# Performance work log

Measured on AMD Instinct MI355X. Metric: run time of the kernel, lower is better.

Reference implementation:

```python
import jax, jax.numpy as jnp
import numpy as np
from jax import lax

SEQ_LEN = 5000
C_IN = 12
KERNEL_LEN = 9
NUM_KERNELS = 10000
BATCH = 16


def _get_dilations(seq_len, kernel_length):
    max_d = (seq_len - 1) // (kernel_length - 1)
    d, out = 1, []
    while d <= max_d:
        out.append(d)
        d *= 2
    return out if out else [1]

DILATIONS = _get_dilations(SEQ_LEN, KERNEL_LEN)  # [1,2,...,512], 10 dilations
KPD = NUM_KERNELS // len(DILATIONS)              # 1000 kernels per dilation


def setup_inputs() -> dict:
    key = jax.random.key(0)
    kx, kw, kb = jax.random.split(key, 3)
    x = jax.random.normal(kx, (BATCH, C_IN, SEQ_LEN), dtype=jnp.float32)
    # ternary {-1,0,1} MiniRocket weights, one [KPD, C_IN, 9] bank per dilation
    weights = jax.random.randint(kw, (len(DILATIONS), KPD, C_IN, KERNEL_LEN), -1, 2).astype(jnp.float32)
    biases = jax.random.normal(kb, (len(DILATIONS), KPD), dtype=jnp.float32) * 0.1
    return {"x": x, "weights": weights, "biases": biases}


def reference(x, weights, biases):
    # x: [B, C_in, L]; weights: [D, KPD, C_in, 9]; biases: [D, KPD]
    feats = []
    for i, d in enumerate(DILATIONS):
        # 'same' padding: total pad = d*(9-1) = 8d (even), split 4d/4d -> SAME
        out = lax.conv_general_dilated(
            x, weights[i],
            window_strides=(1,), padding='SAME', rhs_dilation=(d,),
            dimension_numbers=('NCH', 'OIH', 'NCH'))  # [B, KPD, L]
        maxv = out.max(axis=-1)                                        # [B, KPD]
        ppv = (out > biases[i][None, :, None]).astype(x.dtype).mean(axis=-1)  # [B, KPD]
        feats.append(maxv)
        feats.append(ppv)
    return jnp.concatenate(feats, axis=1)  # [B, 2*NUM_KERNELS]
```

## Files before the change

### kernel.cpp

```cpp
#include <hip/hip_runtime.h>
#include <cstdint>
#include <cstddef>

#define SEQ 5000
#define CIN 12
#define KL 9
#define ND 10
#define KPD 1000
#define NB 16
#define KPAD 128
#define NKP 1024
#define BM 64
#define SPB 79
#define STRIP_US (BM * KPAD)
#define QS 20

typedef __attribute__((ext_vector_type(4))) float f32x4;
typedef __attribute__((ext_vector_type(8))) __bf16 bf16x8;
typedef __attribute__((ext_vector_type(8))) unsigned short u16x8;

__device__ __forceinline__ unsigned fkey(float f) {
    unsigned u = __float_as_uint(f);
    return (u & 0x80000000u) ? ~u : (u | 0x80000000u);
}
__device__ __forceinline__ float unfkey(unsigned k) {
    unsigned u = (k & 0x80000000u) ? (k ^ 0x80000000u) : ~k;
    return __uint_as_float(u);
}
__device__ __forceinline__ unsigned short f2bf(float f) {
    unsigned u = __float_as_uint(f);
    u += 0x7fffu + ((u >> 16) & 1u);
    return (unsigned short)(u >> 16);
}

__global__ __launch_bounds__(256) void wprep(const float* __restrict__ w,
                                             unsigned short* __restrict__ wbf) {
    const int i = blockIdx.x * 256 + threadIdx.x;
    if (i >= ND * NKP * KPAD) return;
    const int kk   = i & (KPAD - 1);
    const int krow = (i >> 7) & (NKP - 1);
    const int di   = i >> 17;
    float v = 0.f;
    if (krow < KPD && kk < CIN * KL)
        v = w[((size_t)di * KPD + krow) * (CIN * KL) + kk];
    wbf[i] = f2bf(v);
}

__global__ __launch_bounds__(256) void im2col(const float* __restrict__ x,
                                              unsigned short* __restrict__ Aim,
                                              int g0) {
    const int s  = blockIdx.x;
    const int b  = blockIdx.y;
    const int dl = blockIdx.z;
    const int d  = 1 << (g0 + dl);
    const int tid  = threadIdx.x;
    const int lane = tid & 63;
    const int wv   = tid >> 6;

    __shared__ __align__(16) unsigned short sb[STRIP_US];

    const float* xb = x + (size_t)b * CIN * SEQ;
    const int t0 = s * BM;
    const int t  = t0 + lane;
    const int base = t - 4 * d;
    const bool rowvalid = (t < SEQ);

#pragma unroll
    for (int cwi = 0; cwi < 4; ++cwi) {
        const int cw = wv * 4 + cwi;
        u16x8 pk;
        int cc = cw * 8;
        int c = cc / 9, j = cc - c * 9;
#pragma unroll
        for (int e = 0; e < 8; ++e) {
            const int idx = base + j * d;
            float v = 0.f;
            if (rowvalid && cc < CIN * KL && idx >= 0 && idx < SEQ)
                v = xb[c * SEQ + idx];
            pk[e] = f2bf(v);
            ++cc; if (++j == KL) { j = 0; ++c; }
        }
        *(u16x8*)(sb + lane * KPAD + ((cw * 8) ^ ((lane & 7) << 3))) = pk;
    }
    __syncthreads();

    unsigned short* outp = Aim + ((size_t)(dl * NB + b) * SPB + s) * STRIP_US;
#pragma unroll
    for (int i = 0; i < 4; ++i) {
        const int u = (i * 256 + tid) * 8;
        *(u16x8*)(outp + u) = *(const u16x8*)(sb + u);
    }
}

__global__ __launch_bounds__(256, 4) void mr_gemm(
    const unsigned short* __restrict__ Aim,
    const unsigned short* __restrict__ wbf,
    const float* __restrict__ bias,
    unsigned* __restrict__ gkey, unsigned* __restrict__ gcnt, int g0)
{
    __shared__ __align__(16) unsigned short lA[2][STRIP_US];

    const int phys = blockIdx.x;
    const int gg   = ((phys >> 6) << 3) | (phys & 7);
    const int ksub = (phys >> 3) & 7;
    const int q  = gg & 3;
    const int b  = (gg >> 2) & 15;
    const int dl = gg >> 6;
    const int di = g0 + dl;

    const int tid  = threadIdx.x;
    const int lane = tid & 63;
    const int wv   = tid >> 6;
    const int wm   = wv >> 1;
    const int wn   = wv & 1;
    const int fr   = lane & 15;
    const int ks   = lane >> 4;

    const int sBeg = q * QS;
    const int sEnd = (q == 3) ? SPB : (sBeg + QS);

    const unsigned short* Ab = Aim + (size_t)(dl * NB + b) * SPB * STRIP_US;
    const unsigned short* wd = wbf + (size_t)di * NKP * KPAD;
    const int kcb = ksub * 128 + wn * 64 + fr;
    const unsigned short* wp = wd + (size_t)kcb * KPAD + ks * 8;
    const float* bb = bias + (size_t)di * KPD;

    float bv[4];
#pragma unroll
    for (int n = 0; n < 4; ++n) {
        const int kc = kcb + n * 16;
        bv[n] = (kc < KPD) ? bb[kc] : 3.0e38f;
    }

    bf16x8 bfr[4][4];
#pragma unroll
    for (int n = 0; n < 4; ++n)
#pragma unroll
        for (int kk = 0; kk < 4; ++kk)
            bfr[n][kk] = *(const bf16x8*)(wp + (size_t)(n * 16) * KPAD + kk * 32);

    float rmax[4];
    unsigned rcnt[4];
#pragma unroll
    for (int n = 0; n < 4; ++n) { rmax[n] = -3.0e38f; rcnt[n] = 0; }

    int abase[2];
#pragma unroll
    for (int m2 = 0; m2 < 2; ++m2) {
        const int row = wm * 32 + m2 * 16 + fr;
        abase[m2] = row * 256 + ((ks * 16) ^ ((row & 7) << 4));
    }

    {
        const char* src = (const char*)(Ab + (size_t)sBeg * STRIP_US) + wv * 4096 + lane * 16;
        char* dst = (char*)&lA[0][0] + wv * 4096;
#pragma unroll
        for (int i = 0; i < 4; ++i)
            __builtin_amdgcn_global_load_lds(
                (const __attribute__((address_space(1))) unsigned int*)(src + i * 1024),
                (__attribute__((address_space(3))) unsigned int*)(dst + i * 1024),
                16, 0, 0);
    }
    __syncthreads();

    for (int s = sBeg; s < sEnd; ++s) {
        const int cur = (s - sBeg) & 1;
        if (s + 1 < sEnd) {
            const char* src = (const char*)(Ab + (size_t)(s + 1) * STRIP_US) + wv * 4096 + lane * 16;
            char* dst = (char*)&lA[cur ^ 1][0] + wv * 4096;
#pragma unroll
            for (int i = 0; i < 4; ++i)
                __builtin_amdgcn_global_load_lds(
                    (const __attribute__((address_space(1))) unsigned int*)(src + i * 1024),
                    (__attribute__((address_space(3))) unsigned int*)(dst + i * 1024),
                    16, 0, 0);
        }

        const char* bufc = (const char*)&lA[cur][0];
        f32x4 acc[2][4];
#pragma unroll
        for (int m2 = 0; m2 < 2; ++m2)
#pragma unroll
            for (int n = 0; n < 4; ++n)
                acc[m2][n] = (f32x4){0.f, 0.f, 0.f, 0.f};

#pragma unroll
        for (int m2 = 0; m2 < 2; ++m2) {
            const char* pa0 = bufc + abase[m2];
            const char* pa1 = bufc + (abase[m2] ^ 64);
#pragma unroll
            for (int kk = 0; kk < 4; ++kk) {
                const char* p = (kk & 1) ? pa1 : pa0;
                const bf16x8 a = *(const bf16x8*)(p + (kk >> 1) * 128);
#pragma unroll
                for (int n = 0; n < 4; ++n)
                    acc[m2][n] = __builtin_amdgcn_mfma_f32_16x16x32_bf16(
                        a, bfr[n][kk], acc[m2][n], 0, 0, 0);
            }
        }

        if (s != SPB - 1) {
#pragma unroll
            for (int n = 0; n < 4; ++n) {
                float m0 = -3.0e38f;
                unsigned c0 = 0;
#pragma unroll
                for (int m2 = 0; m2 < 2; ++m2) {
#pragma unroll
                    for (int r = 0; r < 4; ++r) {
                        const float x0 = acc[m2][n][r];
                        m0 = fmaxf(m0, x0);
                        c0 += (x0 > bv[n]) ? 1u : 0u;
                    }
                }
                rmax[n] = fmaxf(rmax[n], m0);
                rcnt[n] += c0;
            }
        } else {
            if (wm == 0 && ks < 2) {
#pragma unroll
                for (int n = 0; n < 4; ++n) {
#pragma unroll
                    for (int r = 0; r < 4; ++r) {
                        const float x0 = acc[0][n][r];
                        rmax[n] = fmaxf(rmax[n], x0);
                        rcnt[n] += (x0 > bv[n]) ? 1u : 0u;
                    }
                }
            }
        }
        __syncthreads();
    }

#pragma unroll
    for (int n = 0; n < 4; ++n) {
        rmax[n] = fmaxf(rmax[n], __shfl_xor(rmax[n], 16, 64));
        rcnt[n] += (unsigned)__shfl_xor((int)rcnt[n], 16, 64);
        rmax[n] = fmaxf(rmax[n], __shfl_xor(rmax[n], 32, 64));
        rcnt[n] += (unsigned)__shfl_xor((int)rcnt[n], 32, 64);
    }

    if (lane < 16) {
        const size_t slotbase = ((size_t)b * ND + di) * KPD;
#pragma unroll
        for (int n = 0; n < 4; ++n) {
            const int kc = kcb + n * 16;
            if (kc < KPD) {
                atomicMax(&gkey[slotbase + kc], fkey(rmax[n]));
                atomicAdd(&gcnt[slotbase + kc], rcnt[n]);
            }
        }
    }
}

__global__ __launch_bounds__(256) void mr_fin(
    const unsigned* __restrict__ gkey, const unsigned* __restrict__ gcnt,
    float* __restrict__ out)
{
    const int i = blockIdx.x * 256 + threadIdx.x;
    if (i >= NB * ND * KPD) return;
    const int k  = i % KPD;
    const int di = (i / KPD) % ND;
    const int b  = i / (KPD * ND);
    const float maxv = unfkey(gkey[i]);
    const float ppv  = (float)gcnt[i] * (1.0f / (float)SEQ);
    float* ob = out + (size_t)b * (2 * ND * KPD);
    ob[di * 2 * KPD + k]       = maxv;
    ob[di * 2 * KPD + KPD + k] = ppv;
}

extern "C" void kernel_launch(void* const* d_in, const int* in_sizes, int n_in,
                              void* d_out, int out_size, void* d_ws, size_t ws_size,
                              hipStream_t stream) {
    const float* x    = (const float*)d_in[0];
    const float* w    = (const float*)d_in[1];
    const float* bias = (const float*)d_in[2];
    float* out = (float*)d_out;

    const size_t statsB = (size_t)NB * ND * KPD * 4;
    const size_t wbfB   = (size_t)ND * NKP * KPAD * 2;
    unsigned* gkey = (unsigned*)d_ws;
    unsigned* gcnt = (unsigned*)((char*)d_ws + statsB);
    unsigned short* wbf = (unsigned short*)((char*)d_ws + 2 * statsB);
    unsigned short* Aim = (unsigned short*)((char*)d_ws + 2 * statsB + wbfB);

    const size_t perDil = (size_t)NB * SPB * STRIP_US * 2;
    const size_t head = 2 * statsB + wbfB;
    size_t avail = (ws_size > head) ? (ws_size - head) : 0;
    int NG = (int)(avail / perDil);
    if (NG > ND) NG = ND;
    if (NG < 1) NG = 1;

    hipMemsetAsync(d_ws, 0, 2 * statsB, stream);

    const int wtot = ND * NKP * KPAD;
    wprep<<<(wtot + 255) / 256, 256, 0, stream>>>(w, wbf);

    for (int g0 = 0; g0 < ND; g0 += NG) {
        const int ng = (ND - g0 < NG) ? (ND - g0) : NG;
        im2col<<<dim3(SPB, NB, ng), 256, 0, stream>>>(x, Aim, g0);
        mr_gemm<<<ng * 512, 256, 0, stream>>>(Aim, wbf, bias, gkey, gcnt, g0);
    }

    const int tot = NB * ND * KPD;
    mr_fin<<<(tot + 255) / 256, 256, 0, stream>>>(gkey, gcnt, out);
}
```

Measured before the change: 276.5 us.

## Process two A strips per iteration with larger per-wave tiles, reload weights per step

The GEMM loop now stages 128-row superstrips of 32 KB instead of 64-row strips. Each wave computes 64 rows by 64 kernels using 4x4 MFMA accumulators, which raises A-fragment reuse and halves the number of loop iterations and barriers. To save registers, the bf16 weight fragments are no longer kept in registers for the whole kernel and are reloaded from global memory at every k-step. Occupancy hints drop from 4 to 2 blocks per CU. The final superstrip reads past the last real strip, so the workspace head is padded; the exchange is extra weight-load traffic and lower occupancy for better MFMA density.

Result: slower. 323.0 us (+16.8%).

```diff
diff --git a/kernel.cpp b/kernel.cpp
--- a/kernel.cpp
+++ b/kernel.cpp
@@ -13,7 +13,9 @@
 #define BM 64
 #define SPB 79
 #define STRIP_US (BM * KPAD)
-#define QS 20
+#define SS_BYTES 32768
+#define NSS 40
+#define QSS 10
 
 typedef __attribute__((ext_vector_type(4))) float f32x4;
 typedef __attribute__((ext_vector_type(8))) __bf16 bf16x8;
@@ -92,13 +94,13 @@
     }
 }
 
-__global__ __launch_bounds__(256, 4) void mr_gemm(
+__global__ __launch_bounds__(256, 2) void mr_gemm(
     const unsigned short* __restrict__ Aim,
     const unsigned short* __restrict__ wbf,
     const float* __restrict__ bias,
     unsigned* __restrict__ gkey, unsigned* __restrict__ gcnt, int g0)
 {
-    __shared__ __align__(16) unsigned short lA[2][STRIP_US];
+    __shared__ __align__(16) unsigned short lA[2][SS_BYTES / 2];
 
     const int phys = blockIdx.x;
     const int gg   = ((phys >> 6) << 3) | (phys & 7);
@@ -116,10 +118,10 @@
     const int fr   = lane & 15;
     const int ks   = lane >> 4;
 
-    const int sBeg = q * QS;
-    const int sEnd = (q == 3) ? SPB : (sBeg + QS);
-
-    const unsigned short* Ab = Aim + (size_t)(dl * NB + b) * SPB * STRIP_US;
+    const int sBeg = q * QSS;
+    const int sEnd = sBeg + QSS;
+
+    const char* Ab = (const char*)(Aim + (size_t)(dl * NB + b) * SPB * STRIP_US);
     const unsigned short* wd = wbf + (size_t)di * NKP * KPAD;
     const int kcb = ksub * 128 + wn * 64 + fr;
     const unsigned short* wp = wd + (size_t)kcb * KPAD + ks * 8;
@@ -132,80 +134,78 @@
         bv[n] = (kc < KPD) ? bb[kc] : 3.0e38f;
     }
 
-    bf16x8 bfr[4][4];
-#pragma unroll
-    for (int n = 0; n < 4; ++n)
-#pragma unroll
-        for (int kk = 0; kk < 4; ++kk)
-            bfr[n][kk] = *(const bf16x8*)(wp + (size_t)(n * 16) * KPAD + kk * 32);
-
     float rmax[4];
     unsigned rcnt[4];
 #pragma unroll
     for (int n = 0; n < 4; ++n) { rmax[n] = -3.0e38f; rcnt[n] = 0; }
 
-    int abase[2];
-#pragma unroll
-    for (int m2 = 0; m2 < 2; ++m2) {
-        const int row = wm * 32 + m2 * 16 + fr;
+    int abase[4];
+#pragma unroll
+    for (int m2 = 0; m2 < 4; ++m2) {
+        const int row = wm * 64 + m2 * 16 + fr;
         abase[m2] = row * 256 + ((ks * 16) ^ ((row & 7) << 4));
     }
 
     {
-        const char* src = (const char*)(Ab + (size_t)sBeg * STRIP_US) + wv * 4096 + lane * 16;
-        char* dst = (char*)&lA[0][0] + wv * 4096;
-#pragma unroll
-        for (int i = 0; i < 4; ++i)
+        const char* src = Ab + (size_t)sBeg * SS_BYTES + wv * 1024 + lane * 16;
+        char* dst = (char*)&lA[0][0] + wv * 1024;
+#pragma unroll
+        for (int i = 0; i < 8; ++i)
             __builtin_amdgcn_global_load_lds(
-                (const __attribute__((address_space(1))) unsigned int*)(src + i * 1024),
-                (__attribute__((address_space(3))) unsigned int*)(dst + i * 1024),
+                (const __attribute__((address_space(1))) unsigned int*)(src + i * 4096),
+                (__attribute__((address_space(3))) unsigned int*)(dst + i * 4096),
                 16, 0, 0);
     }
     __syncthreads();
 
-    for (int s = sBeg; s < sEnd; ++s) {
-        const int cur = (s - sBeg) & 1;
-        if (s + 1 < sEnd) {
-            const char* src = (const char*)(Ab + (size_t)(s + 1) * STRIP_US) + wv * 4096 + lane * 16;
-            char* dst = (char*)&lA[cur ^ 1][0] + wv * 4096;
-#pragma unroll
-            for (int i = 0; i < 4; ++i)
+    for (int ss = sBeg; ss < sEnd; ++ss) {
+        const int cur = (ss - sBeg) & 1;
+        if (ss + 1 < sEnd) {
+            const char* src = Ab + (size_t)(ss + 1) * SS_BYTES + wv * 1024 + lane * 16;
+            char* dst = (char*)&lA[cur ^ 1][0] + wv * 1024;
+#pragma unroll
+            for (int i = 0; i < 8; ++i)
                 __builtin_amdgcn_global_load_lds(
-                    (const __attribute__((address_space(1))) unsigned int*)(src + i * 1024),
-                    (__attribute__((address_space(3))) unsigned int*)(dst + i * 1024),
+                    (const __attribute__((address_space(1))) unsigned int*)(src + i * 4096),
+                    (__attribute__((address_space(3))) unsigned int*)(dst + i * 4096),
                     16, 0, 0);
         }
 
         const char* bufc = (const char*)&lA[cur][0];
-        f32x4 acc[2][4];
-#pragma unroll
-        for (int m2 = 0; m2 < 2; ++m2)
+        f32x4 acc[4][4];
+#pragma unroll
+        for (int m2 = 0; m2 < 4; ++m2)
 #pragma unroll
             for (int n = 0; n < 4; ++n)
                 acc[m2][n] = (f32x4){0.f, 0.f, 0.f, 0.f};
 
 #pragma unroll
-        for (int m2 = 0; m2 < 2; ++m2) {
-            const char* pa0 = bufc + abase[m2];
-            const char* pa1 = bufc + (abase[m2] ^ 64);
-#pragma unroll
-            for (int kk = 0; kk < 4; ++kk) {
-                const char* p = (kk & 1) ? pa1 : pa0;
-                const bf16x8 a = *(const bf16x8*)(p + (kk >> 1) * 128);
+        for (int kk = 0; kk < 4; ++kk) {
+            bf16x8 bf[4];
+#pragma unroll
+            for (int n = 0; n < 4; ++n)
+                bf[n] = *(const bf16x8*)(wp + (size_t)(n * 16) * KPAD + kk * 32);
+            bf16x8 af[4];
+#pragma unroll
+            for (int m2 = 0; m2 < 4; ++m2) {
+                const int ab = (kk & 1) ? (abase[m2] ^ 64) : abase[m2];
+                af[m2] = *(const bf16x8*)(bufc + ab + (kk >> 1) * 128);
+            }
+#pragma unroll
+            for (int m2 = 0; m2 < 4; ++m2)
 #pragma unroll
                 for (int n = 0; n < 4; ++n)
                     acc[m2][n] = __builtin_amdgcn_mfma_f32_16x16x32_bf16(
-                        a, bfr[n][kk], acc[m2][n], 0, 0, 0);
-            }
-        }
-
-        if (s != SPB - 1) {
+                        af[m2], bf[n], acc[m2][n], 0, 0, 0);
+        }
+
+        if (ss != NSS - 1) {
 #pragma unroll
             for (int n = 0; n < 4; ++n) {
                 float m0 = -3.0e38f;
                 unsigned c0 = 0;
 #pragma unroll
-                for (int m2 = 0; m2 < 2; ++m2) {
+                for (int m2 = 0; m2 < 4; ++m2) {
 #pragma unroll
                     for (int r = 0; r < 4; ++r) {
                         const float x0 = acc[m2][n][r];
@@ -285,7 +285,7 @@
     unsigned short* Aim = (unsigned short*)((char*)d_ws + 2 * statsB + wbfB);
 
     const size_t perDil = (size_t)NB * SPB * STRIP_US * 2;
-    const size_t head = 2 * statsB + wbfB;
+    const size_t head = 2 * statsB + wbfB + 16384;
     size_t avail = (ws_size > head) ? (ws_size - head) : 0;
     int NG = (int)(avail / perDil);
     if (NG > ND) NG = ND;
```
